# Performance work log

Hardware: AMD Instinct MI355X
Metric: run time of the kernel (lower is better)

Reference implementation:

```python
import jax, jax.numpy as jnp
import numpy as np

D = 256; H = 8; HD = D // H; L = 6; NQ = 100; DFF = 2048
FREQS = np.geomspace(1.0, 512.0, 10).astype(np.float32)  # WorldSpacePE: 10 freqs up to 512


def _ln(x, g, b, eps=1e-5):
    m = x.mean(-1, keepdims=True)
    v = ((x - m) ** 2).mean(-1, keepdims=True)
    return (x - m) * jax.lax.rsqrt(v + eps) * g + b


def _mha(q, k, v, Wq, bq, Wk, bk, Wv, bv, Wo, bo, bias=None):
    # standard nn.MultiheadAttention math (batch_first, eval mode -> no dropout)
    B, Q, _ = q.shape; N = k.shape[1]
    qh = (q @ Wq + bq).reshape(B, Q, H, HD).transpose(0, 2, 1, 3)
    kh = (k @ Wk + bk).reshape(B, N, H, HD).transpose(0, 2, 1, 3)
    vh = (v @ Wv + bv).reshape(B, N, H, HD).transpose(0, 2, 1, 3)
    s = jnp.einsum('bhqd,bhkd->bhqk', qh, kh) / np.float32(np.sqrt(HD))
    if bias is not None:
        s = s + bias
    a = jax.nn.softmax(s, axis=-1)
    o = jnp.einsum('bhqk,bhkd->bhqd', a, vh).transpose(0, 2, 1, 3).reshape(B, Q, D)
    return o @ Wo + bo


def setup_inputs() -> dict:
    key = jax.random.key(0)
    cnt = [0]
    def nk():
        cnt[0] += 1
        return jax.random.fold_in(key, cnt[0])
    def rn(shape, scale=0.02):
        return (jax.random.normal(nk(), shape) * scale).astype(jnp.float32)
    def zeros(shape):
        return jnp.zeros(shape, jnp.float32)
    def ones(shape):
        return jnp.ones(shape, jnp.float32)
    B, N, NT = 8, 4096, 32
    inp = {
        'image_feats': jax.random.normal(nk(), (B, N, D), jnp.float32),
        'text_feats': jax.random.normal(nk(), (B, NT, 256), jnp.float32),
        'pointmap': jax.random.normal(nk(), (B, N, 3), jnp.float32),
        'query_embed': rn((NQ, D)),
        'presence_tok': rn((1, D)),
        'text_proj_W': rn((256, D)), 'text_proj_b': zeros((D,)),
        'tWq': rn((D, D)), 'tbq': zeros((D,)), 'tWk': rn((D, D)), 'tbk': zeros((D,)),
        'tWv': rn((D, D)), 'tbv': zeros((D,)), 'tWo': rn((D, D)), 'tbo': zeros((D,)),
        'tln_g': ones((D,)), 'tln_b': zeros((D,)),
        'wpe_W': rn((60, D)), 'wpe_b': zeros((D,)),
        'sa_Wq': rn((L, D, D)), 'sa_bq': zeros((L, D)), 'sa_Wk': rn((L, D, D)), 'sa_bk': zeros((L, D)),
        'sa_Wv': rn((L, D, D)), 'sa_bv': zeros((L, D)), 'sa_Wo': rn((L, D, D)), 'sa_bo': zeros((L, D)),
        'ca_Wq': rn((L, D, D)), 'ca_bq': zeros((L, D)), 'ca_Wk': rn((L, D, D)), 'ca_bk': zeros((L, D)),
        'ca_Wv': rn((L, D, D)), 'ca_bv': zeros((L, D)), 'ca_Wo': rn((L, D, D)), 'ca_bo': zeros((L, D)),
        'ffn_W1': rn((L, D, DFF)), 'ffn_b1': zeros((L, DFF)),
        'ffn_W2': rn((L, DFF, D)), 'ffn_b2': zeros((L, D)),
        'ln1_g': ones((L, D)), 'ln1_b': zeros((L, D)),
        'ln2_g': ones((L, D)), 'ln2_b': zeros((L, D)),
        'ln3_g': ones((L, D)), 'ln3_b': zeros((L, D)),
        'pos_W': rn((L, D, 3)), 'pos_b': zeros((L, 3)),
        'beta': ones((L, H)),  # gasa_beta_init = 1.0
        'fin_g': ones((D,)), 'fin_b': zeros((D,)),
        'pW1': rn((D, D)), 'pb1': zeros((D,)),
        'pW2': rn((D, D)), 'pb2': zeros((D,)),
        'pW3': rn((D, 1)), 'pb3': zeros((1,)),
    }
    return inp


def reference(image_feats, text_feats, pointmap, query_embed, presence_tok,
              text_proj_W, text_proj_b,
              tWq, tbq, tWk, tbk, tWv, tbv, tWo, tbo, tln_g, tln_b,
              wpe_W, wpe_b,
              sa_Wq, sa_bq, sa_Wk, sa_bk, sa_Wv, sa_bv, sa_Wo, sa_bo,
              ca_Wq, ca_bq, ca_Wk, ca_bk, ca_Wv, ca_bv, ca_Wo, ca_bo,
              ffn_W1, ffn_b1, ffn_W2, ffn_b2,
              ln1_g, ln1_b, ln2_g, ln2_b, ln3_g, ln3_b,
              pos_W, pos_b, beta, fin_g, fin_b,
              pW1, pb1, pW2, pb2, pW3, pb3):
    B, N, _ = image_feats.shape
    # --- world-space PE from pointmap (sin/cos over 10 freqs, 3 coords -> 60d -> D) ---
    ang = pointmap[..., None] * jnp.asarray(FREQS)            # [B,N,3,10]
    enc = jnp.concatenate([jnp.sin(ang), jnp.cos(ang)], -1).reshape(B, N, 60)
    mem = image_feats + enc @ wpe_W + wpe_b                   # PE added to memory
    # --- text conditioning of queries ---
    txt = text_feats @ text_proj_W + text_proj_b              # [B,NT,D]
    x = jnp.concatenate([
        jnp.broadcast_to(query_embed, (B, NQ, D)),
        jnp.broadcast_to(presence_tok, (B, 1, D)),
    ], axis=1)                                                # [B,101,D]
    x = _ln(x + _mha(x, txt, txt, tWq, tbq, tWk, tbk, tWv, tbv, tWo, tbo), tln_g, tln_b)
    # --- decoder layers with GASA geometric attention bias (post-norm) ---
    for i in range(L):
        x = _ln(x + _mha(x, x, x, sa_Wq[i], sa_bq[i], sa_Wk[i], sa_bk[i],
                         sa_Wv[i], sa_bv[i], sa_Wo[i], sa_bo[i]), ln1_g[i], ln1_b[i])
        pos_q = x @ pos_W[i] + pos_b[i]                       # [B,101,3] predicted 3D pos
        d2 = jnp.sum((pos_q[:, :, None, :] - pointmap[:, None, :, :]) ** 2, -1)  # [B,101,N]
        bias = -jax.nn.softplus(beta[i])[None, :, None, None] * d2[:, None]      # [B,H,101,N]
        x = _ln(x + _mha(x, mem, mem, ca_Wq[i], ca_bq[i], ca_Wk[i], ca_bk[i],
                         ca_Wv[i], ca_bv[i], ca_Wo[i], ca_bo[i], bias=bias), ln2_g[i], ln2_b[i])
        h = jax.nn.relu(x @ ffn_W1[i] + ffn_b1[i]) @ ffn_W2[i] + ffn_b2[i]
        x = _ln(x + h, ln3_g[i], ln3_b[i])
    x = _ln(x, fin_g, fin_b)
    hs = x[:, :NQ]                                            # [B,100,D]
    pres = x[:, NQ]                                           # [B,D]
    h = jax.nn.relu(pres @ pW1 + pb1)
    h = jax.nn.relu(h @ pW2 + pb2)
    presence_logit = h @ pW3 + pb3                            # [B,1]
    return hs, presence_logit
```

## Files before the change

kernel.cpp:

```cpp
#include <hip/hip_runtime.h>
#include <math.h>

#define DD 256
#define NH 8
#define HDIM 32
#define NLAY 6
#define NQRY 100
#define TT 101
#define BB 8
#define NN 4096
#define NTXT 32
#define FFD 2048
#define MM (BB*TT)
#define MMP 896
#define BNN (BB*NN)
#define KC 8
#define KPC (NN/KC)
#define D2 (DD*DD)
#define C1S 0.25506807170842403f

typedef __bf16 bf16x8 __attribute__((ext_vector_type(8)));
typedef float f32x4v __attribute__((ext_vector_type(4)));
typedef unsigned int u32x4 __attribute__((ext_vector_type(4)));
typedef unsigned int u32x2 __attribute__((ext_vector_type(2)));

__device__ __forceinline__ ushort f2b(float f) {
  unsigned u = __builtin_bit_cast(unsigned, f);
  u += 0x7FFF + ((u >> 16) & 1);
  return (ushort)(u >> 16);
}
__device__ __forceinline__ unsigned pk2(float lo, float hi) {
  return (unsigned)f2b(lo) | ((unsigned)f2b(hi) << 16);
}
__device__ __forceinline__ f32x4v mfma16(bf16x8 a, bf16x8 b, f32x4v c) {
  return __builtin_amdgcn_mfma_f32_16x16x32_bf16(a, b, c, 0, 0, 0);
}

__device__ __forceinline__ void gemm_core(const ushort* __restrict__ A, size_t lda,
                                          const ushort* __restrict__ Bt, size_t ldb,
                                          int m0, int n0, int kBeg, int kEnd,
                                          char* AsB, char* BsB, int t,
                                          f32x4v acc[2][4]) {
  int w = t >> 6, l = t & 63, lq = l & 15, lg = l >> 4;
  int acol = (t & 7) * 8;
  for (int k0 = kBeg; k0 < kEnd; k0 += 64) {
    __syncthreads();
#pragma unroll
    for (int p = 0; p < 4; ++p) {
      int row = (t >> 3) + p * 32;
      u32x4 v = *(const u32x4*)(A + (size_t)(m0 + row) * lda + k0 + acol);
      *(u32x4*)(AsB + row * 128 + ((acol * 2) ^ ((row & 7) << 4))) = v;
    }
#pragma unroll
    for (int p = 0; p < 2; ++p) {
      int row = (t >> 3) + p * 32;
      u32x4 v = *(const u32x4*)(Bt + (size_t)(n0 + row) * ldb + k0 + acol);
      *(u32x4*)(BsB + row * 128 + ((acol * 2) ^ ((row & 7) << 4))) = v;
    }
    __syncthreads();
#pragma unroll
    for (int ks = 0; ks < 2; ++ks) {
      bf16x8 af[2], bfr[4];
#pragma unroll
      for (int mt = 0; mt < 2; ++mt) {
        int row = w * 32 + mt * 16 + lq;
        int kb = ks * 64 + lg * 16;
        af[mt] = __builtin_bit_cast(
            bf16x8, *(const u32x4*)(AsB + row * 128 + (kb ^ ((row & 7) << 4))));
      }
#pragma unroll
      for (int nt = 0; nt < 4; ++nt) {
        int row = nt * 16 + lq;
        int kb = ks * 64 + lg * 16;
        bfr[nt] = __builtin_bit_cast(
            bf16x8, *(const u32x4*)(BsB + row * 128 + (kb ^ ((row & 7) << 4))));
      }
#pragma unroll
      for (int mt = 0; mt < 2; ++mt)
#pragma unroll
        for (int nt = 0; nt < 4; ++nt) acc[mt][nt] = mfma16(af[mt], bfr[nt], acc[mt][nt]);
    }
  }
}

__global__ __launch_bounds__(256) void k_enc(const float* __restrict__ pm,
                                             ushort* __restrict__ encb) {
  int t = threadIdx.x;
  int row = blockIdx.x * 32 + (t >> 3);
  int kb = (t & 7) * 8;
  ushort o[8];
#pragma unroll
  for (int u = 0; u < 8; ++u) {
    int k = kb + u;
    float val = 0.f;
    if (k < 60) {
      int c = k / 20, jj = k % 20;
      float f = (float)(1 << (jj % 10));
      float a = pm[(size_t)row * 3 + c] * f;
      val = (jj < 10) ? sinf(a) : cosf(a);
    }
    o[u] = f2b(val);
  }
  *(u32x4*)(encb + (size_t)row * 64 + kb) = *(const u32x4*)o;
}

__global__ __launch_bounds__(256) void k_wpet(const float* __restrict__ wpeW,
                                              ushort* __restrict__ wpeT) {
  int n = blockIdx.x * 16 + (threadIdx.x >> 4);
  int k = (threadIdx.x & 15) * 4;
  ushort o[4];
#pragma unroll
  for (int u = 0; u < 4; ++u) {
    int kk = k + u;
    o[u] = (kk < 60) ? f2b(wpeW[(size_t)kk * DD + n]) : (ushort)0;
  }
  *(u32x2*)(wpeT + (size_t)n * 64 + k) = *(const u32x2*)o;
}

__global__ __launch_bounds__(256) void k_gemm_mem(const ushort* __restrict__ encb,
                                                  const ushort* __restrict__ wpeT,
                                                  const float* __restrict__ wpeb,
                                                  const float* __restrict__ img,
                                                  ushort* __restrict__ memb) {
  __shared__ __align__(16) char AsB[16384];
  __shared__ __align__(16) char BsB[8192];
  int m0 = blockIdx.x * 128, n0 = blockIdx.y * 64;
  f32x4v acc[2][4] = {};
  gemm_core(encb, 64, wpeT, 64, m0, n0, 0, 64, AsB, BsB, threadIdx.x, acc);
  int t = threadIdx.x, w = t >> 6, l = t & 63, lq = l & 15, lg = l >> 4;
#pragma unroll
  for (int nt = 0; nt < 4; ++nt) {
    int n = n0 + nt * 16 + lq;
    float bv = wpeb[n];
#pragma unroll
    for (int mt = 0; mt < 2; ++mt) {
      int rowg = m0 + w * 32 + mt * 16 + lg * 4;
      f32x4v a = acc[mt][nt];
#pragma unroll
      for (int r = 0; r < 4; ++r)
        memb[(size_t)(rowg + r) * DD + n] = f2b(a[r] + bv + img[(size_t)(rowg + r) * DD + n]);
    }
  }
}

struct T2BArgs {
  const float* fam[8];
  const float* single[5];
  const float* fW1; const float* fW2;
  ushort* wT; ushort* w1T; ushort* w2T;
};
__global__ __launch_bounds__(256) void k_t2b_all(T2BArgs a) {
  __shared__ ushort T[64][72];
  int id = blockIdx.x;
  const float* src; ushort* dst; int K, N, k0, n0;
  if (id < 768) {
    int fam = id / 96, rem = id % 96, mi = rem >> 4, ti = rem & 15;
    src = a.fam[fam] + (size_t)mi * D2;
    dst = a.wT + (size_t)(fam * 6 + mi) * D2;
    K = DD; N = DD; k0 = (ti >> 2) * 64; n0 = (ti & 3) * 64;
  } else if (id < 848) {
    int j = (id - 768) >> 4, ti = (id - 768) & 15;
    src = a.single[j];
    dst = a.wT + (size_t)(48 + j) * D2;
    K = DD; N = DD; k0 = (ti >> 2) * 64; n0 = (ti & 3) * 64;
  } else if (id < 1616) {
    int t2 = id - 848, mi = t2 >> 7, ti = t2 & 127;
    src = a.fW1 + (size_t)mi * DD * FFD;
    dst = a.w1T + (size_t)mi * DD * FFD;
    K = DD; N = FFD; k0 = (ti >> 5) * 64; n0 = (ti & 31) * 64;
  } else {
    int t2 = id - 1616, mi = t2 >> 7, ti = t2 & 127;
    src = a.fW2 + (size_t)mi * DD * FFD;
    dst = a.w2T + (size_t)mi * DD * FFD;
    K = FFD; N = DD; k0 = (ti >> 2) * 64; n0 = (ti & 3) * 64;
  }
  int t = threadIdx.x;
  int kk = t >> 4, nn4 = (t & 15) * 4;
#pragma unroll
  for (int p = 0; p < 4; ++p) {
    int krow = kk + p * 16;
    float4 v = *(const float4*)(src + (size_t)(k0 + krow) * N + n0 + nn4);
    T[nn4 + 0][krow] = f2b(v.x);
    T[nn4 + 1][krow] = f2b(v.y);
    T[nn4 + 2][krow] = f2b(v.z);
    T[nn4 + 3][krow] = f2b(v.w);
  }
  __syncthreads();
  int nn = t >> 3, kk8 = (t & 7) * 8;
#pragma unroll
  for (int p = 0; p < 2; ++p) {
    int nrow = nn + p * 32;
    u32x4 v = *(const u32x4*)(&T[nrow][kk8]);
    *(u32x4*)(dst + (size_t)(n0 + nrow) * K + k0 + kk8) = v;
  }
}

__global__ __launch_bounds__(256) void k_pm4(const float* __restrict__ pm,
                                             float4* __restrict__ pm4) {
  int i = blockIdx.x * 256 + threadIdx.x;
  float x = pm[(size_t)i * 3 + 0];
  float y = pm[(size_t)i * 3 + 1];
  float z = pm[(size_t)i * 3 + 2];
  float4 v;
  v.x = x; v.y = y; v.z = z; v.w = x * x + y * y + z * z;
  pm4[i] = v;
}

__global__ __launch_bounds__(256) void k_f2b(const float* __restrict__ in,
                                             ushort* __restrict__ out, int n) {
  int i = (blockIdx.x * 256 + threadIdx.x) * 4;
  if (i + 3 < n) {
    float4 v = *(const float4*)(in + i);
    out[i + 0] = f2b(v.x);
    out[i + 1] = f2b(v.y);
    out[i + 2] = f2b(v.z);
    out[i + 3] = f2b(v.w);
  }
}

template <int OM>
__global__ __launch_bounds__(256) void k_gemm_gen(const ushort* __restrict__ A,
                                                  const ushort* __restrict__ Bt,
                                                  const float* __restrict__ bias,
                                                  void* __restrict__ C, int Nc) {
  __shared__ __align__(16) char AsB[16384];
  __shared__ __align__(16) char BsB[8192];
  int m0 = blockIdx.x * 128, n0 = blockIdx.y * 64;
  f32x4v acc[2][4] = {};
  gemm_core(A, 256, Bt, 256, m0, n0, 0, 256, AsB, BsB, threadIdx.x, acc);
  int t = threadIdx.x, w = t >> 6, l = t & 63, lq = l & 15, lg = l >> 4;
#pragma unroll
  for (int nt = 0; nt < 4; ++nt) {
    int n = n0 + nt * 16 + lq;
    float bv = bias[n];
#pragma unroll
    for (int mt = 0; mt < 2; ++mt) {
      int rowg = m0 + w * 32 + mt * 16 + lg * 4;
      f32x4v a = acc[mt][nt];
      a[0] += bv; a[1] += bv; a[2] += bv; a[3] += bv;
      if (OM == 2) {
        a[0] = fmaxf(a[0], 0.f); a[1] = fmaxf(a[1], 0.f);
        a[2] = fmaxf(a[2], 0.f); a[3] = fmaxf(a[3], 0.f);
      }
      if (OM == 3) { a[0] *= C1S; a[1] *= C1S; a[2] *= C1S; a[3] *= C1S; }
      if (OM == 0) {
        float* Cf = (float*)C;
#pragma unroll
        for (int r = 0; r < 4; ++r) Cf[(size_t)(rowg + r) * Nc + n] = a[r];
      } else {
        ushort* Cb = (ushort*)C;
#pragma unroll
        for (int r = 0; r < 4; ++r) Cb[(size_t)(rowg + r) * Nc + n] = f2b(a[r]);
      }
    }
  }
}

__global__ __launch_bounds__(256) void k_gemm_qkv(
    const ushort* __restrict__ A, const ushort* __restrict__ Bq,
    const ushort* __restrict__ Bk, const ushort* __restrict__ Bv,
    const float* __restrict__ bq, const float* __restrict__ bk,
    const float* __restrict__ bv, ushort* __restrict__ Qb,
    ushort* __restrict__ Kbs, ushort* __restrict__ Vst) {
  __shared__ __align__(16) char AsB[16384];
  __shared__ __align__(16) char BsB[8192];
  int sel = blockIdx.y >> 2;
  int n0 = (blockIdx.y & 3) * 64;
  int m0 = blockIdx.x * 128;
  const ushort* Bt = sel == 0 ? Bq : (sel == 1 ? Bk : Bv);
  const float* bias = sel == 0 ? bq : (sel == 1 ? bk : bv);
  f32x4v acc[2][4] = {};
  gemm_core(A, 256, Bt, 256, m0, n0, 0, 256, AsB, BsB, threadIdx.x, acc);
  int t = threadIdx.x, w = t >> 6, l = t & 63, lq = l & 15, lg = l >> 4;
#pragma unroll
  for (int nt = 0; nt < 4; ++nt) {
    int n = n0 + nt * 16 + lq;
    float bvv = bias[n];
#pragma unroll
    for (int mt = 0; mt < 2; ++mt) {
      int rowg = m0 + w * 32 + mt * 16 + lg * 4;
      f32x4v a = acc[mt][nt];
      a[0] += bvv; a[1] += bvv; a[2] += bvv; a[3] += bvv;
      if (sel == 0) {
#pragma unroll
        for (int r = 0; r < 4; ++r) Qb[(size_t)(rowg + r) * DD + n] = f2b(a[r] * C1S);
      } else if (sel == 1) {
#pragma unroll
        for (int r = 0; r < 4; ++r) Kbs[(size_t)(rowg + r) * DD + n] = f2b(a[r]);
      } else {
        int h = n >> 5, dd = n & 31;
#pragma unroll
        for (int r = 0; r < 4; ++r) {
          int rg = rowg + r;
          if (rg < MM) {
            int b = rg / TT, tq = rg % TT;
            Vst[((size_t)((b * 8 + h) * 32 + dd)) * 128 + tq] = f2b(a[r]);
          }
        }
      }
    }
  }
}

template <int QPROJ>
__global__ __launch_bounds__(256) void k_gemm_o_ln(
    const ushort* __restrict__ A, const ushort* __restrict__ WoT,
    const float* __restrict__ bo, const float* __restrict__ xres,
    const float* __restrict__ g, const float* __restrict__ be,
    float* __restrict__ xout, ushort* __restrict__ xbout,
    const float* __restrict__ Wp, const float* __restrict__ bp,
    float* __restrict__ pqout) {
  __shared__ __align__(16) char AsB[8192];
  __shared__ __align__(16) char BsB[32768];
  int m0 = blockIdx.x * 64;
  int t = threadIdx.x, w = t >> 6, l = t & 63, lq = l & 15, lg = l >> 4;
  int acol = (t & 7) * 8;
  f32x4v acc[16] = {};
  for (int k0 = 0; k0 < 256; k0 += 64) {
    __syncthreads();
#pragma unroll
    for (int p = 0; p < 2; ++p) {
      int row = (t >> 3) + p * 32;
      u32x4 v = *(const u32x4*)(A + (size_t)(m0 + row) * 256 + k0 + acol);
      *(u32x4*)(AsB + row * 128 + ((acol * 2) ^ ((row & 7) << 4))) = v;
    }
#pragma unroll
    for (int p = 0; p < 8; ++p) {
      int row = (t >> 3) + p * 32;
      u32x4 v = *(const u32x4*)(WoT + (size_t)row * 256 + k0 + acol);
      *(u32x4*)(BsB + row * 128 + ((acol * 2) ^ ((row & 7) << 4))) = v;
    }
    __syncthreads();
#pragma unroll
    for (int ks = 0; ks < 2; ++ks) {
      int kb = ks * 64 + lg * 16;
      int arow = w * 16 + lq;
      bf16x8 af = __builtin_bit_cast(
          bf16x8, *(const u32x4*)(AsB + arow * 128 + (kb ^ ((arow & 7) << 4))));
#pragma unroll
      for (int nt = 0; nt < 16; ++nt) {
        int brow = nt * 16 + lq;
        bf16x8 bf = __builtin_bit_cast(
            bf16x8, *(const u32x4*)(BsB + brow * 128 + (kb ^ ((brow & 7) << 4))));
        acc[nt] = mfma16(af, bf, acc[nt]);
      }
    }
  }
  int rowb = m0 + w * 16 + lg * 4;
  float s[4] = {}, s2[4] = {};
#pragma unroll
  for (int nt = 0; nt < 16; ++nt) {
    int col = nt * 16 + lq;
    float bv = bo[col];
    f32x4v a = acc[nt];
#pragma unroll
    for (int r = 0; r < 4; ++r) {
      a[r] += bv + xres[(size_t)(rowb + r) * DD + col];
      s[r] += a[r];
      s2[r] += a[r] * a[r];
    }
    acc[nt] = a;
  }
#pragma unroll
  for (int r = 0; r < 4; ++r) {
#pragma unroll
    for (int o = 1; o < 16; o <<= 1) {
      s[r] += __shfl_xor(s[r], o, 64);
      s2[r] += __shfl_xor(s2[r], o, 64);
    }
  }
  float mu[4], inv[4];
#pragma unroll
  for (int r = 0; r < 4; ++r) {
    mu[r] = s[r] * (1.f / DD);
    float var = s2[r] * (1.f / DD) - mu[r] * mu[r];
    inv[r] = rsqrtf(var + 1e-5f);
  }
  float pp0[4] = {}, pp1[4] = {}, pp2[4] = {};
#pragma unroll
  for (int nt = 0; nt < 16; ++nt) {
    int col = nt * 16 + lq;
    float gd = g[col], bd = be[col];
    float w0 = 0.f, w1 = 0.f, w2 = 0.f;
    if (QPROJ) { w0 = Wp[col * 3]; w1 = Wp[col * 3 + 1]; w2 = Wp[col * 3 + 2]; }
#pragma unroll
    for (int r = 0; r < 4; ++r) {
      float ln = (acc[nt][r] - mu[r]) * inv[r] * gd + bd;
      xout[(size_t)(rowb + r) * DD + col] = ln;
      xbout[(size_t)(rowb + r) * DD + col] = f2b(ln);
      if (QPROJ) { pp0[r] += ln * w0; pp1[r] += ln * w1; pp2[r] += ln * w2; }
    }
  }
  if (QPROJ) {
#pragma unroll
    for (int r = 0; r < 4; ++r) {
#pragma unroll
      for (int o = 1; o < 16; o <<= 1) {
        pp0[r] += __shfl_xor(pp0[r], o, 64);
        pp1[r] += __shfl_xor(pp1[r], o, 64);
        pp2[r] += __shfl_xor(pp2[r], o, 64);
      }
      if (lq == 0) {
        pqout[(size_t)(rowb + r) * 3 + 0] = pp0[r] + bp[0];
        pqout[(size_t)(rowb + r) * 3 + 1] = pp1[r] + bp[1];
        pqout[(size_t)(rowb + r) * 3 + 2] = pp2[r] + bp[2];
      }
    }
  }
}

__global__ __launch_bounds__(256) void k_init_x(const float* __restrict__ qe,
                                                const float* __restrict__ pt,
                                                float* __restrict__ x,
                                                ushort* __restrict__ xb) {
  int r = blockIdx.x, d = threadIdx.x;
  int t = r % TT;
  float v = (t < NQRY) ? qe[t * DD + d] : pt[d];
  x[(size_t)r * DD + d] = v;
  xb[(size_t)r * DD + d] = f2b(v);
}

__global__ __launch_bounds__(128) void k_attn_small(const float* __restrict__ q,
                                                    const float* __restrict__ k,
                                                    const float* __restrict__ v,
                                                    ushort* __restrict__ out,
                                                    int NK) {
  int bh = blockIdx.x;
  int b = bh >> 3, h = bh & 7;
  __shared__ float Ks[TT][HDIM];
  __shared__ float Vs[TT][HDIM];
  for (int i = threadIdx.x; i < NK * HDIM; i += 128) {
    int n = i >> 5, j = i & 31;
    Ks[n][j] = k[(size_t)(b * NK + n) * DD + h * HDIM + j];
    Vs[n][j] = v[(size_t)(b * NK + n) * DD + h * HDIM + j];
  }
  __syncthreads();
  int t = threadIdx.x;
  if (t >= TT) return;
  float qv[HDIM];
  const float* qp = q + (size_t)(b * TT + t) * DD + h * HDIM;
#pragma unroll
  for (int j = 0; j < HDIM; ++j) qv[j] = qp[j];
  const float sc = 0.17677669529663687f * 1.4426950408889634f;
  float l = 0.f, acc[HDIM] = {};
  for (int n = 0; n < NK; ++n) {
    float s = 0.f;
#pragma unroll
    for (int j = 0; j < HDIM; ++j) s += qv[j] * Ks[n][j];
    float p = exp2f(s * sc);
    l += p;
#pragma unroll
    for (int j = 0; j < HDIM; ++j) acc[j] += p * Vs[n][j];
  }
  float inv = 1.f / l;
  ushort* op = out + (size_t)(b * TT + t) * DD + h * HDIM;
#pragma unroll
  for (int j = 0; j < HDIM; ++j) op[j] = f2b(acc[j] * inv);
}

__global__ __launch_bounds__(256) void k_self_mfma(const ushort* __restrict__ Qb,
                                                   const ushort* __restrict__ Kbs,
                                                   const ushort* __restrict__ Vst,
                                                   ushort* __restrict__ out) {
  int bh = blockIdx.x;
  int b = bh >> 3, h = bh & 7;
  int t = threadIdx.x, w = t >> 6, l = t & 63, lq = l & 15, lg = l >> 4;
  __shared__ ushort Plds[4][2][16][40];
  const f32x4v Z = {0.f, 0.f, 0.f, 0.f};
  bf16x8 qfb[2];
  f32x4v oacc[2][2] = {};
  float lsum[2] = {0.f, 0.f};
#pragma unroll
  for (int qi = 0; qi < 2; ++qi) {
    int qidx = (w * 2 + qi) * 16 + lq;
    int qc = qidx < TT ? qidx : TT - 1;
    qfb[qi] = __builtin_bit_cast(
        bf16x8, *(const u32x4*)(Qb + (size_t)(b * TT + qc) * DD + h * HDIM + lg * 8));
  }
  for (int kk = 0; kk < 128; kk += 32) {
    bf16x8 kf[2], vf[2];
#pragma unroll
    for (int t2 = 0; t2 < 2; ++t2) {
      int key = kk + t2 * 16 + lq;
      int kc2 = key < TT ? key : TT - 1;
      kf[t2] = __builtin_bit_cast(
          bf16x8, *(const u32x4*)(Kbs + (size_t)(b * TT + kc2) * DD + h * HDIM + lg * 8));
    }
#pragma unroll
    for (int dt = 0; dt < 2; ++dt)
      vf[dt] = __builtin_bit_cast(
          bf16x8, *(const u32x4*)(Vst + (size_t)(bh * 32 + dt * 16 + lq) * 128 + kk + lg * 8));
#pragma unroll
    for (int qi = 0; qi < 2; ++qi) {
      f32x4v s0 = mfma16(kf[0], qfb[qi], Z);
      f32x4v s1 = mfma16(kf[1], qfb[qi], Z);
      float p[2][4];
#pragma unroll
      for (int t2 = 0; t2 < 2; ++t2) {
#pragma unroll
        for (int r = 0; r < 4; ++r) {
          int kr = kk + t2 * 16 + lg * 4 + r;
          float sv = (t2 == 0) ? s0[r] : s1[r];
          p[t2][r] = (kr < TT) ? exp2f(sv) : 0.f;
        }
        lsum[qi] += (p[t2][0] + p[t2][1]) + (p[t2][2] + p[t2][3]);
      }
      u32x2 w0, w1;
      w0[0] = pk2(p[0][0], p[0][1]);
      w0[1] = pk2(p[0][2], p[0][3]);
      w1[0] = pk2(p[1][0], p[1][1]);
      w1[1] = pk2(p[1][2], p[1][3]);
      *(u32x2*)(&Plds[w][qi][lq][lg * 4]) = w0;
      *(u32x2*)(&Plds[w][qi][lq][16 + lg * 4]) = w1;
      bf16x8 pf = __builtin_bit_cast(bf16x8, *(const u32x4*)(&Plds[w][qi][lq][lg * 8]));
      oacc[qi][0] = mfma16(vf[0], pf, oacc[qi][0]);
      oacc[qi][1] = mfma16(vf[1], pf, oacc[qi][1]);
    }
  }
#pragma unroll
  for (int qi = 0; qi < 2; ++qi) {
    float lv = lsum[qi];
    lv += __shfl_xor(lv, 16, 64);
    lv += __shfl_xor(lv, 32, 64);
    float inv = 1.f / lv;
    int qidx = (w * 2 + qi) * 16 + lq;
    if (qidx < TT) {
      ushort* op = out + (size_t)(b * TT + qidx) * DD + h * HDIM;
#pragma unroll
      for (int dt = 0; dt < 2; ++dt)
#pragma unroll
        for (int r = 0; r < 4; ++r)
          op[dt * 16 + lg * 4 + r] = f2b(oacc[qi][dt][r] * inv);
    }
  }
}

__global__ __launch_bounds__(256) void k_gemm_kv(const ushort* __restrict__ A,
                                                 const ushort* __restrict__ Btk,
                                                 const ushort* __restrict__ Btv,
                                                 const float* __restrict__ bk,
                                                 const float* __restrict__ bv,
                                                 ushort* __restrict__ Kb,
                                                 ushort* __restrict__ Vt) {
  __shared__ __align__(16) char LB[34816];
  char* AsB = LB;
  char* BsB = LB + 16384;
  int isV = blockIdx.y >= 2;
  int n0 = (blockIdx.y & 1) * 128;
  int m0 = blockIdx.x * 128;
  const ushort* Bt = isV ? Btv : Btk;
  int t = threadIdx.x, w = t >> 6, l = t & 63, lq = l & 15, lg = l >> 4;
  int acol = (t & 7) * 8;
  f32x4v acc[2][8] = {};
  for (int k0 = 0; k0 < 256; k0 += 64) {
    __syncthreads();
#pragma unroll
    for (int p = 0; p < 4; ++p) {
      int row = (t >> 3) + p * 32;
      u32x4 va = *(const u32x4*)(A + (size_t)(m0 + row) * 256 + k0 + acol);
      *(u32x4*)(AsB + row * 128 + ((acol * 2) ^ ((row & 7) << 4))) = va;
      u32x4 vb = *(const u32x4*)(Bt + (size_t)(n0 + row) * 256 + k0 + acol);
      *(u32x4*)(BsB + row * 128 + ((acol * 2) ^ ((row & 7) << 4))) = vb;
    }
    __syncthreads();
#pragma unroll
    for (int ks = 0; ks < 2; ++ks) {
      int kb = ks * 64 + lg * 16;
      bf16x8 af[2], bfr[8];
#pragma unroll
      for (int mt = 0; mt < 2; ++mt) {
        int row = w * 32 + mt * 16 + lq;
        af[mt] = __builtin_bit_cast(
            bf16x8, *(const u32x4*)(AsB + row * 128 + (kb ^ ((row & 7) << 4))));
      }
#pragma unroll
      for (int nt = 0; nt < 8; ++nt) {
        int row = nt * 16 + lq;
        bfr[nt] = __builtin_bit_cast(
            bf16x8, *(const u32x4*)(BsB + row * 128 + (kb ^ ((row & 7) << 4))));
      }
#pragma unroll
      for (int mt = 0; mt < 2; ++mt)
#pragma unroll
        for (int nt = 0; nt < 8; ++nt) acc[mt][nt] = mfma16(af[mt], bfr[nt], acc[mt][nt]);
    }
  }
  if (!isV) {
#pragma unroll
    for (int nt = 0; nt < 8; ++nt) {
      int n = n0 + nt * 16 + lq;
      float bvv = bk[n];
#pragma unroll
      for (int mt = 0; mt < 2; ++mt) {
        int rowg = m0 + w * 32 + mt * 16 + lg * 4;
        f32x4v a = acc[mt][nt];
#pragma unroll
        for (int r = 0; r < 4; ++r) Kb[(size_t)(rowg + r) * DD + n] = f2b(a[r] + bvv);
      }
    }
  } else {
    ushort* T = (ushort*)LB;
    __syncthreads();
#pragma unroll
    for (int nt = 0; nt < 8; ++nt) {
      int ddl = nt * 16 + lq;
      float bvv = bv[n0 + ddl];
#pragma unroll
      for (int mt = 0; mt < 2; ++mt) {
        int kl = w * 32 + mt * 16 + lg * 4;
        f32x4v a = acc[mt][nt];
        u32x2 pv;
        pv[0] = pk2(a[0] + bvv, a[1] + bvv);
        pv[1] = pk2(a[2] + bvv, a[3] + bvv);
        *(u32x2*)(T + ddl * 136 + kl) = pv;
      }
    }
    __syncthreads();
    int row = t >> 1, half = t & 1;
    int b = m0 >> 12, key0 = m0 & 4095;
    const ushort* src = T + row * 136 + half * 64;
    ushort* dst = Vt + ((size_t)(b * 256 + n0 + row)) * 4096 + key0 + half * 64;
#pragma unroll
    for (int i = 0; i < 8; ++i)
      *(u32x4*)(dst + i * 8) = *(const u32x4*)(src + i * 8);
  }
}

__global__ __launch_bounds__(256) void k_ffn2sk(const ushort* __restrict__ A,
                                                const ushort* __restrict__ Bt,
                                                float* __restrict__ P) {
  __shared__ __align__(16) char AsB[16384];
  __shared__ __align__(16) char BsB[8192];
  int m0 = blockIdx.x * 128, n0 = blockIdx.y * 64, z = blockIdx.z;
  f32x4v acc[2][4] = {};
  gemm_core(A, FFD, Bt, FFD, m0, n0, z * 256, z * 256 + 256, AsB, BsB, threadIdx.x, acc);
  int t = threadIdx.x, w = t >> 6, l = t & 63, lq = l & 15, lg = l >> 4;
#pragma unroll
  for (int nt = 0; nt < 4; ++nt) {
    int n = n0 + nt * 16 + lq;
#pragma unroll
    for (int mt = 0; mt < 2; ++mt) {
      int rowg = m0 + w * 32 + mt * 16 + lg * 4;
      f32x4v a = acc[mt][nt];
#pragma unroll
      for (int r = 0; r < 4; ++r)
        P[((size_t)z * MMP + rowg + r) * DD + n] = a[r];
    }
  }
}

__global__ __launch_bounds__(256) void k_red_ln3(const float* __restrict__ P,
                                                 const float* __restrict__ bias,
                                                 const float* __restrict__ xres,
                                                 const float* __restrict__ g,
                                                 const float* __restrict__ be,
                                                 float* __restrict__ xout,
                                                 ushort* __restrict__ xbout) {
  int row = blockIdx.x, d = threadIdx.x;
  float a = xres[(size_t)row * DD + d] + bias[d];
#pragma unroll
  for (int z = 0; z < 8; ++z) a += P[((size_t)z * MMP + row) * DD + d];
  float s = a, s2 = a * a;
#pragma unroll
  for (int o = 1; o < 64; o <<= 1) {
    s += __shfl_xor(s, o, 64);
    s2 += __shfl_xor(s2, o, 64);
  }
  __shared__ float ws[4], ws2[4];
  int wid = d >> 6;
  if ((d & 63) == 0) { ws[wid] = s; ws2[wid] = s2; }
  __syncthreads();
  s = ws[0] + ws[1] + ws[2] + ws[3];
  s2 = ws2[0] + ws2[1] + ws2[2] + ws2[3];
  float m = s * (1.f / DD);
  float var = s2 * (1.f / DD) - m * m;
  float inv = rsqrtf(var + 1e-5f);
  float r_ = (a - m) * inv * g[d] + be[d];
  xout[(size_t)row * DD + d] = r_;
  xbout[(size_t)row * DD + d] = f2b(r_);
}

__global__ __launch_bounds__(256) void k_cross_mfma(
    const ushort* __restrict__ Qb, const ushort* __restrict__ Kb,
    const ushort* __restrict__ Vt, const float* __restrict__ posq,
    const float4* __restrict__ pm4, const float* __restrict__ betaL,
    float* __restrict__ pacc, float* __restrict__ pl) {
  int bh = blockIdx.x, kc = blockIdx.y;
  int b = bh >> 3, h = bh & 7;
  int t = threadIdx.x, w = t >> 6, l = t & 63, lq = l & 15, lg = l >> 4;
  const float L2E = 1.4426950408889634f;
  float spb = log1pf(expf(betaL[h]));
  float cb = spb * L2E;

  __shared__ float4 pm4s[KPC];
  __shared__ ushort Plds[4][2][16][40];

  int kbase = b * NN + kc * KPC;
  for (int i = t; i < KPC; i += 256) pm4s[i] = pm4[kbase + i];
  __syncthreads();

  const f32x4v Z = {0.f, 0.f, 0.f, 0.f};
  bf16x8 qfb[2];
  float a0[2], px[2], py[2], pz[2];
  f32x4v oacc[2][2] = {};
  float lsum[2] = {0.f, 0.f};

#pragma unroll
  for (int qi = 0; qi < 2; ++qi) {
    int qt = w * 2 + qi;
    int qidx = qt * 16 + lq;
    int qc = qidx < TT ? qidx : TT - 1;
    size_t xr = (size_t)(b * TT + qc);
    qfb[qi] = __builtin_bit_cast(
        bf16x8, *(const u32x4*)(Qb + xr * 256 + h * 32 + lg * 8));
    float qx = posq[xr * 3 + 0], qy = posq[xr * 3 + 1], qz = posq[xr * 3 + 2];
    a0[qi] = -cb * (qx * qx + qy * qy + qz * qz);
    px[qi] = 2.f * cb * qx;
    py[qi] = 2.f * cb * qy;
    pz[qi] = 2.f * cb * qz;
  }

  for (int kk = 0; kk < KPC; kk += 32) {
    bf16x8 kf[2], vf[2];
#pragma unroll
    for (int t2 = 0; t2 < 2; ++t2)
      kf[t2] = __builtin_bit_cast(
          bf16x8, *(const u32x4*)(Kb + (size_t)(kbase + kk + t2 * 16 + lq) * 256 +
                                  h * 32 + lg * 8));
#pragma unroll
    for (int dt = 0; dt < 2; ++dt)
      vf[dt] = __builtin_bit_cast(
          bf16x8, *(const u32x4*)(Vt + (size_t)(bh * 32 + dt * 16 + lq) * 4096 +
                                  kc * KPC + kk + lg * 8));
    float bx[2][4], by[2][4], bz[2][4], b0[2][4];
#pragma unroll
    for (int t2 = 0; t2 < 2; ++t2)
#pragma unroll
      for (int r = 0; r < 4; ++r) {
        float4 pv = pm4s[kk + t2 * 16 + lg * 4 + r];
        bx[t2][r] = pv.x; by[t2][r] = pv.y; bz[t2][r] = pv.z;
        b0[t2][r] = cb * pv.w;
      }
#pragma unroll
    for (int qi = 0; qi < 2; ++qi) {
      f32x4v s0 = mfma16(kf[0], qfb[qi], Z);
      f32x4v s1 = mfma16(kf[1], qfb[qi], Z);
      float p[2][4];
#pragma unroll
      for (int t2 = 0; t2 < 2; ++t2) {
#pragma unroll
        for (int r = 0; r < 4; ++r) {
          float sv = (t2 == 0) ? s0[r] : s1[r];
          float bias = fmaf(px[qi], bx[t2][r],
                       fmaf(py[qi], by[t2][r],
                       fmaf(pz[qi], bz[t2][r], a0[qi] - b0[t2][r])));
          p[t2][r] = exp2f(sv + bias);
        }
        lsum[qi] += (p[t2][0] + p[t2][1]) + (p[t2][2] + p[t2][3]);
      }
      u32x2 w0, w1;
      w0[0] = pk2(p[0][0], p[0][1]);
      w0[1] = pk2(p[0][2], p[0][3]);
      w1[0] = pk2(p[1][0], p[1][1]);
      w1[1] = pk2(p[1][2], p[1][3]);
      *(u32x2*)(&Plds[w][qi][lq][lg * 4]) = w0;
      *(u32x2*)(&Plds[w][qi][lq][16 + lg * 4]) = w1;
      bf16x8 pf = __builtin_bit_cast(bf16x8, *(const u32x4*)(&Plds[w][qi][lq][lg * 8]));
      oacc[qi][0] = mfma16(vf[0], pf, oacc[qi][0]);
      oacc[qi][1] = mfma16(vf[1], pf, oacc[qi][1]);
    }
  }

#pragma unroll
  for (int qi = 0; qi < 2; ++qi) {
    float lv = lsum[qi];
    lv += __shfl_xor(lv, 16, 64);
    lv += __shfl_xor(lv, 32, 64);
// ... 45 lines not shown
  }
  __shared__ float ws[4], ws2[4];
  int wid = d >> 6;
  if ((d & 63) == 0) { ws[wid] = s; ws2[wid] = s2; }
  __syncthreads();
  s = ws[0] + ws[1] + ws[2] + ws[3];
  s2 = ws2[0] + ws2[1] + ws2[2] + ws2[3];
  float m = s * (1.f / DD);
  float var = s2 * (1.f / DD) - m * m;
  float inv = rsqrtf(var + 1e-5f);
  float r = (v - m) * inv * g[d] + be[d];
  if (tq < NQRY) hs[((size_t)(b * NQRY + tq)) * DD + d] = r;
  else pres[(size_t)b * DD + d] = r;
}

__global__ __launch_bounds__(256) void k_mlp8(const float* __restrict__ in,
                                              const float* __restrict__ W,
                                              const float* __restrict__ b,
                                              float* __restrict__ out) {
  __shared__ float ins[8][DD];
  __shared__ float red[8][32][8];
  int t = threadIdx.x;
  for (int i = t; i < 8 * DD; i += 256) ins[i >> 8][i & 255] = in[i];
  __syncthreads();
  int c = t & 31, ks = t >> 5;
  int cg = blockIdx.x * 32 + c;
  float acc[8] = {};
  for (int k = ks * 32; k < ks * 32 + 32; ++k) {
    float w = W[(size_t)k * DD + cg];
#pragma unroll
    for (int r = 0; r < 8; ++r) acc[r] += ins[r][k] * w;
  }
#pragma unroll
  for (int r = 0; r < 8; ++r) red[ks][c][r] = acc[r];
  __syncthreads();
  int c2 = t & 31, r2 = t >> 5;
  float s = 0.f;
#pragma unroll
  for (int k2 = 0; k2 < 8; ++k2) s += red[k2][c2][r2];
  s = fmaxf(s + b[blockIdx.x * 32 + c2], 0.f);
  out[(size_t)r2 * DD + blockIdx.x * 32 + c2] = s;
}

__global__ __launch_bounds__(256) void k_logit(const float* __restrict__ h2,
                                               const float* __restrict__ W3,
                                               const float* __restrict__ b3,
                                               float* __restrict__ out) {
  int r = threadIdx.x >> 5, lane = threadIdx.x & 31;
  float s = 0.f;
  for (int k = lane; k < DD; k += 32) s += h2[r * DD + k] * W3[k];
#pragma unroll
  for (int o = 16; o; o >>= 1) s += __shfl_xor(s, o, 32);
  if (lane == 0) out[r] = s + b3[0];
}

extern "C" void kernel_launch(void* const* d_in, const int* in_sizes, int n_in,
                              void* d_out, int out_size, void* d_ws, size_t ws_size,
                              hipStream_t stream) {
  (void)in_sizes; (void)n_in; (void)out_size; (void)ws_size;
  auto F = [&](int i) { return (const float*)d_in[i]; };
  const float* img   = F(0);
  const float* txtf  = F(1);
  const float* pm    = F(2);
  const float* qe    = F(3);
  const float* ptok  = F(4);
  const float* tpW   = F(5);
  const float* tpb   = F(6);
  const float* tWq   = F(7);  const float* tbq = F(8);
  const float* tWk   = F(9);  const float* tbk = F(10);
  const float* tWv   = F(11); const float* tbv = F(12);
  const float* tWo   = F(13); const float* tbo = F(14);
  const float* tlng  = F(15); const float* tlnb = F(16);
  const float* wpeW  = F(17); const float* wpeb = F(18);
  const float* saWq  = F(19); const float* sabq = F(20);
  const float* saWk  = F(21); const float* sabk = F(22);
  const float* saWv  = F(23); const float* sabv = F(24);
  const float* saWo  = F(25); const float* sabo = F(26);
  const float* caWq  = F(27); const float* cabq = F(28);
  const float* caWk  = F(29); const float* cabk = F(30);
  const float* caWv  = F(31); const float* cabv = F(32);
  const float* caWo  = F(33); const float* cabo = F(34);
  const float* fW1   = F(35); const float* fb1 = F(36);
  const float* fW2   = F(37); const float* fb2 = F(38);
  const float* ln1g  = F(39); const float* ln1b = F(40);
  const float* ln2g  = F(41); const float* ln2b = F(42);
  const float* ln3g  = F(43); const float* ln3b = F(44);
  const float* posW  = F(45); const float* posb = F(46);
  const float* beta  = F(47);
  const float* fing  = F(48); const float* finb = F(49);
  const float* pW1   = F(50); const float* pb1 = F(51);
  const float* pW2   = F(52); const float* pb2 = F(53);
  const float* pW3   = F(54); const float* pb3 = F(55);

  char* wp = (char*)d_ws;
  auto alloc = [&](size_t bytes) {
    char* p = wp;
    wp += (bytes + 255) & ~(size_t)255;
    return (void*)p;
  };
  ushort* memb = (ushort*)alloc((size_t)BNN * DD * 2);
  ushort* Kb   = (ushort*)alloc((size_t)BNN * DD * 2);
  ushort* Vt   = (ushort*)alloc((size_t)64 * 32 * 4096 * 2);
  ushort* encb = (ushort*)alloc((size_t)BNN * 64 * 2);
  ushort* wT   = (ushort*)alloc((size_t)53 * D2 * 2);
  ushort* w1T  = (ushort*)alloc((size_t)6 * FFD * DD * 2);
  ushort* w2T  = (ushort*)alloc((size_t)6 * DD * FFD * 2);
  ushort* xb   = (ushort*)alloc((size_t)MMP * DD * 2);
  ushort* hb   = (ushort*)alloc((size_t)MMP * FFD * 2);
  ushort* tDb  = (ushort*)alloc((size_t)MMP * DD * 2);
  ushort* tQb  = (ushort*)alloc((size_t)MMP * DD * 2);
  ushort* tKb  = (ushort*)alloc((size_t)MMP * DD * 2);
  ushort* tQb2 = (ushort*)alloc((size_t)MMP * DD * 2);
  ushort* Vst  = (ushort*)alloc((size_t)64 * 32 * 128 * 2);
  ushort* txtb = (ushort*)alloc((size_t)BB * NTXT * DD * 2);
  ushort* txtb2= (ushort*)alloc((size_t)BB * NTXT * DD * 2);
  float* fp2  = (float*)alloc((size_t)8 * MMP * DD * 4);
  float* x    = (float*)alloc((size_t)MMP * DD * 4);
  float* tA   = (float*)alloc((size_t)MMP * DD * 4);
  float* tK   = (float*)alloc((size_t)BB * NTXT * DD * 4);
  float* tV   = (float*)alloc((size_t)BB * NTXT * DD * 4);
  float* pacc = (float*)alloc((size_t)(KC * 64 + 8) * TT * HDIM * 4);
  float* pl   = (float*)alloc((size_t)(KC * 64 + 8) * TT * 4);
  float* posq = (float*)alloc((size_t)4096 * 4);
  float4* pm4 = (float4*)alloc((size_t)BNN * 16);
  float* pres = (float*)alloc((size_t)BB * DD * 4);
  float* ph1  = (float*)alloc((size_t)BB * DD * 4);
  float* ph2  = (float*)alloc((size_t)BB * DD * 4);
  ushort* wpeT = (ushort*)alloc((size_t)DD * 64 * 2);

  k_enc<<<BNN / 32, 256, 0, stream>>>(pm, encb);
  k_wpet<<<16, 256, 0, stream>>>(wpeW, wpeT);
  k_pm4<<<BNN / 256, 256, 0, stream>>>(pm, pm4);
  T2BArgs ta;
  ta.fam[0] = saWq; ta.fam[1] = saWk; ta.fam[2] = saWv; ta.fam[3] = saWo;
  ta.fam[4] = caWq; ta.fam[5] = caWk; ta.fam[6] = caWv; ta.fam[7] = caWo;
  ta.single[0] = tpW; ta.single[1] = tWq; ta.single[2] = tWk;
  ta.single[3] = tWv; ta.single[4] = tWo;
  ta.fW1 = fW1; ta.fW2 = fW2; ta.wT = wT; ta.w1T = w1T; ta.w2T = w2T;
  k_t2b_all<<<2384, 256, 0, stream>>>(ta);
  k_gemm_mem<<<dim3(256, 4), 256, 0, stream>>>(encb, wpeT, wpeb, img, memb);

  k_f2b<<<(BB * NTXT * DD) / 1024, 256, 0, stream>>>(txtf, txtb, BB * NTXT * DD);
  k_gemm_gen<1><<<dim3(2, 4), 256, 0, stream>>>(txtb, wT + (size_t)48 * D2, tpb, txtb2, DD);
  k_gemm_gen<0><<<dim3(2, 4), 256, 0, stream>>>(txtb2, wT + (size_t)50 * D2, tbk, tK, DD);
  k_gemm_gen<0><<<dim3(2, 4), 256, 0, stream>>>(txtb2, wT + (size_t)51 * D2, tbv, tV, DD);
  k_init_x<<<MM, 256, 0, stream>>>(qe, ptok, x, xb);
  k_gemm_gen<0><<<dim3(7, 4), 256, 0, stream>>>(xb, wT + (size_t)49 * D2, tbq, tA, DD);
  k_attn_small<<<64, 128, 0, stream>>>(tA, tK, tV, tDb, NTXT);
  k_gemm_o_ln<0><<<14, 256, 0, stream>>>(tDb, wT + (size_t)52 * D2, tbo, x, tlng, tlnb,
                                         x, xb, nullptr, nullptr, nullptr);

  for (int i = 0; i < NLAY; ++i) {
    int iD = i * DD;
    k_gemm_qkv<<<dim3(7, 12), 256, 0, stream>>>(
        xb, wT + (size_t)(0 + i) * D2, wT + (size_t)(6 + i) * D2, wT + (size_t)(12 + i) * D2,
        sabq + iD, sabk + iD, sabv + iD, tQb, tKb, Vst);
    k_self_mfma<<<64, 256, 0, stream>>>(tQb, tKb, Vst, tDb);
    k_gemm_o_ln<1><<<14, 256, 0, stream>>>(tDb, wT + (size_t)(18 + i) * D2, sabo + iD,
                                           x, ln1g + iD, ln1b + iD, x, xb,
                                           posW + (size_t)i * DD * 3, posb + i * 3, posq);
    k_gemm_gen<3><<<dim3(7, 4), 256, 0, stream>>>(xb, wT + (size_t)(24 + i) * D2,
                                                  cabq + iD, tQb2, DD);
    k_gemm_kv<<<dim3(256, 4), 256, 0, stream>>>(memb, wT + (size_t)(30 + i) * D2,
                                                wT + (size_t)(36 + i) * D2,
                                                cabk + iD, cabv + iD, Kb, Vt);
    k_cross_mfma<<<dim3(64, KC), 256, 0, stream>>>(tQb2, Kb, Vt, posq, pm4,
                                                   beta + i * NH, pacc, pl);
    k_cross_merge<<<dim3(64, 13), 256, 0, stream>>>(pacc, pl, tDb);
    k_gemm_o_ln<0><<<14, 256, 0, stream>>>(tDb, wT + (size_t)(42 + i) * D2, cabo + iD,
                                           x, ln2g + iD, ln2b + iD, x, xb,
                                           nullptr, nullptr, nullptr);
    k_gemm_gen<2><<<dim3(7, 32), 256, 0, stream>>>(xb, w1T + (size_t)i * DD * FFD,
                                                   fb1 + i * FFD, hb, FFD);
    k_ffn2sk<<<dim3(7, 4, 8), 256, 0, stream>>>(hb, w2T + (size_t)i * DD * FFD, fp2);
    k_red_ln3<<<MM, 256, 0, stream>>>(fp2, fb2 + iD, x, ln3g + iD, ln3b + iD, x, xb);
  }

  k_fin<<<MM, 256, 0, stream>>>(x, fing, finb, (float*)d_out, pres);
  k_mlp8<<<8, 256, 0, stream>>>(pres, pW1, pb1, ph1);
  k_mlp8<<<8, 256, 0, stream>>>(ph1, pW2, pb2, ph2);
  k_logit<<<1, 256, 0, stream>>>(ph2, pW3, pb3, (float*)d_out + (size_t)BB * NQRY * DD);
}
```

Measured before the change: 858.1 us.

## Use direct global-to-LDS loads and merge self-QKV with cross K/V GEMM launch

GEMM tile staging now uses global_load_lds 16-byte async loads with the XOR swizzle applied on the source address, avoiding the round trip through registers. The self-attention QKV projection and the per-layer memory K/V projection are fused into one kernel launch whose block index selects the role. The memory K/V work is independent of x, so it fills the GPU alongside the small QKV GEMM and removes one launch per layer. This adds reliance on the gfx950 LDS-direct load path and a heterogeneous kernel with shared LDS sizing.

```diff
diff --git a/kernel.cpp b/kernel.cpp
--- a/kernel.cpp
+++ b/kernel.cpp
@@ -36,27 +36,39 @@
   return __builtin_amdgcn_mfma_f32_16x16x32_bf16(a, b, c, 0, 0, 0);
 }
 
+__device__ __forceinline__ void gload16(const void* g, void* l) {
+  __builtin_amdgcn_global_load_lds(
+      (const __attribute__((address_space(1))) void*)g,
+      (__attribute__((address_space(3))) void*)l, 16, 0, 0);
+}
+
+template <int NROWS>
+__device__ __forceinline__ void stage_sw(const ushort* __restrict__ G, size_t ldg,
+                                         int row0, int k0, char* lds, int w, int l) {
+  constexpr int RPW = NROWS / 4;
+  constexpr int ISSUES = RPW / 8;
+#pragma unroll
+  for (int p = 0; p < ISSUES; ++p) {
+    int slot = p * 64 + l;
+    int row = w * RPW + (slot >> 3);
+    int blk = slot & 7;
+    int cb = blk ^ (row & 7);
+    const ushort* src = G + (size_t)(row0 + row) * ldg + (size_t)k0 + cb * 8;
+    char* db = lds + (w * RPW + p * 8) * 128;
+    gload16(src, db);
+  }
+}
+
 __device__ __forceinline__ void gemm_core(const ushort* __restrict__ A, size_t lda,
                                           const ushort* __restrict__ Bt, size_t ldb,
                                           int m0, int n0, int kBeg, int kEnd,
                                           char* AsB, char* BsB, int t,
                                           f32x4v acc[2][4]) {
   int w = t >> 6, l = t & 63, lq = l & 15, lg = l >> 4;
-  int acol = (t & 7) * 8;
   for (int k0 = kBeg; k0 < kEnd; k0 += 64) {
     __syncthreads();
-#pragma unroll
-    for (int p = 0; p < 4; ++p) {
-      int row = (t >> 3) + p * 32;
-      u32x4 v = *(const u32x4*)(A + (size_t)(m0 + row) * lda + k0 + acol);
-      *(u32x4*)(AsB + row * 128 + ((acol * 2) ^ ((row & 7) << 4))) = v;
-    }
-#pragma unroll
-    for (int p = 0; p < 2; ++p) {
-      int row = (t >> 3) + p * 32;
-      u32x4 v = *(const u32x4*)(Bt + (size_t)(n0 + row) * ldb + k0 + acol);
-      *(u32x4*)(BsB + row * 128 + ((acol * 2) ^ ((row & 7) << 4))) = v;
-    }
+    stage_sw<128>(A, lda, m0, k0, AsB, w, l);
+    stage_sw<64>(Bt, ldb, n0, k0, BsB, w, l);
     __syncthreads();
 #pragma unroll
     for (int ks = 0; ks < 2; ++ks) {
@@ -256,48 +268,133 @@
   }
 }
 
-__global__ __launch_bounds__(256) void k_gemm_qkv(
-    const ushort* __restrict__ A, const ushort* __restrict__ Bq,
+__global__ __launch_bounds__(256) void k_qkv_kv(
+    const ushort* __restrict__ xbA, const ushort* __restrict__ Bq,
     const ushort* __restrict__ Bk, const ushort* __restrict__ Bv,
     const float* __restrict__ bq, const float* __restrict__ bk,
     const float* __restrict__ bv, ushort* __restrict__ Qb,
-    ushort* __restrict__ Kbs, ushort* __restrict__ Vst) {
-  __shared__ __align__(16) char AsB[16384];
-  __shared__ __align__(16) char BsB[8192];
-  int sel = blockIdx.y >> 2;
-  int n0 = (blockIdx.y & 3) * 64;
-  int m0 = blockIdx.x * 128;
-  const ushort* Bt = sel == 0 ? Bq : (sel == 1 ? Bk : Bv);
-  const float* bias = sel == 0 ? bq : (sel == 1 ? bk : bv);
-  f32x4v acc[2][4] = {};
-  gemm_core(A, 256, Bt, 256, m0, n0, 0, 256, AsB, BsB, threadIdx.x, acc);
+    ushort* __restrict__ Kbs, ushort* __restrict__ Vst,
+    const ushort* __restrict__ memb, const ushort* __restrict__ Btk,
+    const ushort* __restrict__ Btv, const float* __restrict__ cbk,
+    const float* __restrict__ cbv, ushort* __restrict__ Kb,
+    ushort* __restrict__ Vt) {
+  __shared__ __align__(16) char LB[34816];
+  int bid = blockIdx.x;
   int t = threadIdx.x, w = t >> 6, l = t & 63, lq = l & 15, lg = l >> 4;
-#pragma unroll
-  for (int nt = 0; nt < 4; ++nt) {
-    int n = n0 + nt * 16 + lq;
-    float bvv = bias[n];
-#pragma unroll
-    for (int mt = 0; mt < 2; ++mt) {
-      int rowg = m0 + w * 32 + mt * 16 + lg * 4;
-      f32x4v a = acc[mt][nt];
-      a[0] += bvv; a[1] += bvv; a[2] += bvv; a[3] += bvv;
-      if (sel == 0) {
-#pragma unroll
-        for (int r = 0; r < 4; ++r) Qb[(size_t)(rowg + r) * DD + n] = f2b(a[r] * C1S);
-      } else if (sel == 1) {
-#pragma unroll
-        for (int r = 0; r < 4; ++r) Kbs[(size_t)(rowg + r) * DD + n] = f2b(a[r]);
-      } else {
-        int h = n >> 5, dd = n & 31;
-#pragma unroll
-        for (int r = 0; r < 4; ++r) {
-          int rg = rowg + r;
-          if (rg < MM) {
-            int b = rg / TT, tq = rg % TT;
-            Vst[((size_t)((b * 8 + h) * 32 + dd)) * 128 + tq] = f2b(a[r]);
+  if (bid < 84) {
+    char* AsB = LB;
+    char* BsB = LB + 16384;
+    int m0 = (bid % 7) * 128;
+    int yy = bid / 7;
+    int sel = yy >> 2;
+    int n0 = (yy & 3) * 64;
+    const ushort* Bt = sel == 0 ? Bq : (sel == 1 ? Bk : Bv);
+    const float* bias = sel == 0 ? bq : (sel == 1 ? bk : bv);
+    f32x4v acc[2][4] = {};
+    gemm_core(xbA, 256, Bt, 256, m0, n0, 0, 256, AsB, BsB, t, acc);
+#pragma unroll
+    for (int nt = 0; nt < 4; ++nt) {
+      int n = n0 + nt * 16 + lq;
+      float bvv = bias[n];
+#pragma unroll
+      for (int mt = 0; mt < 2; ++mt) {
+        int rowg = m0 + w * 32 + mt * 16 + lg * 4;
+        f32x4v a = acc[mt][nt];
+        a[0] += bvv; a[1] += bvv; a[2] += bvv; a[3] += bvv;
+        if (sel == 0) {
+#pragma unroll
+          for (int r = 0; r < 4; ++r) Qb[(size_t)(rowg + r) * DD + n] = f2b(a[r] * C1S);
+        } else if (sel == 1) {
+#pragma unroll
+          for (int r = 0; r < 4; ++r) Kbs[(size_t)(rowg + r) * DD + n] = f2b(a[r]);
+        } else {
+          int h = n >> 5, dd = n & 31;
+#pragma unroll
+          for (int r = 0; r < 4; ++r) {
+            int rg = rowg + r;
+            if (rg < MM) {
+              int b = rg / TT, tq = rg % TT;
+              Vst[((size_t)((b * 8 + h) * 32 + dd)) * 128 + tq] = f2b(a[r]);
+            }
           }
         }
       }
+    }
+  } else {
+    char* AsB = LB;
+    char* BsB = LB + 16384;
+    int tile = bid - 84;
+    int m0 = (tile & 255) * 128;
+    int yy = tile >> 8;
+    int isV = yy >= 2;
+    int n0 = (yy & 1) * 128;
+    const ushort* Bt = isV ? Btv : Btk;
+    f32x4v acc[2][8] = {};
+    for (int k0 = 0; k0 < 256; k0 += 64) {
+      __syncthreads();
+      stage_sw<128>(memb, 256, m0, k0, AsB, w, l);
+      stage_sw<128>(Bt, 256, n0, k0, BsB, w, l);
+      __syncthreads();
+#pragma unroll
+      for (int ks = 0; ks < 2; ++ks) {
+        int kb = ks * 64 + lg * 16;
+        bf16x8 af[2], bfr[8];
+#pragma unroll
+        for (int mt = 0; mt < 2; ++mt) {
+          int row = w * 32 + mt * 16 + lq;
+          af[mt] = __builtin_bit_cast(
+              bf16x8, *(const u32x4*)(AsB + row * 128 + (kb ^ ((row & 7) << 4))));
+        }
+#pragma unroll
+        for (int nt = 0; nt < 8; ++nt) {
+          int row = nt * 16 + lq;
+          bfr[nt] = __builtin_bit_cast(
+              bf16x8, *(const u32x4*)(BsB + row * 128 + (kb ^ ((row & 7) << 4))));
+        }
+#pragma unroll
+        for (int mt = 0; mt < 2; ++mt)
+#pragma unroll
+          for (int nt = 0; nt < 8; ++nt) acc[mt][nt] = mfma16(af[mt], bfr[nt], acc[mt][nt]);
+      }
+    }
+    if (!isV) {
+#pragma unroll
+      for (int nt = 0; nt < 8; ++nt) {
+        int n = n0 + nt * 16 + lq;
+        float bvv = cbk[n];
+#pragma unroll
+        for (int mt = 0; mt < 2; ++mt) {
+          int rowg = m0 + w * 32 + mt * 16 + lg * 4;
+          f32x4v a = acc[mt][nt];
+#pragma unroll
+          for (int r = 0; r < 4; ++r) Kb[(size_t)(rowg + r) * DD + n] = f2b(a[r] + bvv);
+        }
+      }
+    } else {
+      ushort* T = (ushort*)LB;
+      __syncthreads();
+#pragma unroll
+      for (int nt = 0; nt < 8; ++nt) {
+        int ddl = nt * 16 + lq;
+        float bvv = cbv[n0 + ddl];
+#pragma unroll
+        for (int mt = 0; mt < 2; ++mt) {
+          int kl = w * 32 + mt * 16 + lg * 4;
+          f32x4v a = acc[mt][nt];
+          u32x2 pv;
+          pv[0] = pk2(a[0] + bvv, a[1] + bvv);
+          pv[1] = pk2(a[2] + bvv, a[3] + bvv);
+          *(u32x2*)(T + ddl * 136 + kl) = pv;
+        }
+      }
+      __syncthreads();
+      int row = t >> 1, half = t & 1;
+      int b = m0 >> 12, key0 = m0 & 4095;
+      const ushort* src = T + row * 136 + half * 64;
+      ushort* dst = Vt + ((size_t)(b * 256 + n0 + row)) * 4096 + key0 + half * 64;
+#pragma unroll
+      for (int i = 0; i < 8; ++i)
+        *(u32x4*)(dst + i * 8) = *(const u32x4*)(src + i * 8);
     }
   }
 }
@@ -314,22 +411,11 @@
   __shared__ __align__(16) char BsB[32768];
   int m0 = blockIdx.x * 64;
   int t = threadIdx.x, w = t >> 6, l = t & 63, lq = l & 15, lg = l >> 4;
-  int acol = (t & 7) * 8;
   f32x4v acc[16] = {};
   for (int k0 = 0; k0 < 256; k0 += 64) {
     __syncthreads();
-#pragma unroll
-    for (int p = 0; p < 2; ++p) {
-      int row = (t >> 3) + p * 32;
-      u32x4 v = *(const u32x4*)(A + (size_t)(m0 + row) * 256 + k0 + acol);
-      *(u32x4*)(AsB + row * 128 + ((acol * 2) ^ ((row & 7) << 4))) = v;
-    }
-#pragma unroll
-    for (int p = 0; p < 8; ++p) {
-      int row = (t >> 3) + p * 32;
-      u32x4 v = *(const u32x4*)(WoT + (size_t)row * 256 + k0 + acol);
-      *(u32x4*)(BsB + row * 128 + ((acol * 2) ^ ((row & 7) << 4))) = v;
-    }
+    stage_sw<64>(A, 256, m0, k0, AsB, w, l);
+    stage_sw<256>(WoT, 256, 0, k0, BsB, w, l);
     __syncthreads();
 #pragma unroll
     for (int ks = 0; ks < 2; ++ks) {
@@ -532,97 +618,6 @@
         for (int r = 0; r < 4; ++r)
           op[dt * 16 + lg * 4 + r] = f2b(oacc[qi][dt][r] * inv);
     }
-  }
-}
-
-__global__ __launch_bounds__(256) void k_gemm_kv(const ushort* __restrict__ A,
-                                                 const ushort* __restrict__ Btk,
-                                                 const ushort* __restrict__ Btv,
-                                                 const float* __restrict__ bk,
-                                                 const float* __restrict__ bv,
-                                                 ushort* __restrict__ Kb,
-                                                 ushort* __restrict__ Vt) {
-  __shared__ __align__(16) char LB[34816];
-  char* AsB = LB;
-  char* BsB = LB + 16384;
-  int isV = blockIdx.y >= 2;
-  int n0 = (blockIdx.y & 1) * 128;
-  int m0 = blockIdx.x * 128;
-  const ushort* Bt = isV ? Btv : Btk;
-  int t = threadIdx.x, w = t >> 6, l = t & 63, lq = l & 15, lg = l >> 4;
-  int acol = (t & 7) * 8;
-  f32x4v acc[2][8] = {};
-  for (int k0 = 0; k0 < 256; k0 += 64) {
-    __syncthreads();
-#pragma unroll
-    for (int p = 0; p < 4; ++p) {
-      int row = (t >> 3) + p * 32;
-      u32x4 va = *(const u32x4*)(A + (size_t)(m0 + row) * 256 + k0 + acol);
-      *(u32x4*)(AsB + row * 128 + ((acol * 2) ^ ((row & 7) << 4))) = va;
-      u32x4 vb = *(const u32x4*)(Bt + (size_t)(n0 + row) * 256 + k0 + acol);
-      *(u32x4*)(BsB + row * 128 + ((acol * 2) ^ ((row & 7) << 4))) = vb;
-    }
-    __syncthreads();
-#pragma unroll
-    for (int ks = 0; ks < 2; ++ks) {
-      int kb = ks * 64 + lg * 16;
-      bf16x8 af[2], bfr[8];
-#pragma unroll
-      for (int mt = 0; mt < 2; ++mt) {
-        int row = w * 32 + mt * 16 + lq;
-        af[mt] = __builtin_bit_cast(
-            bf16x8, *(const u32x4*)(AsB + row * 128 + (kb ^ ((row & 7) << 4))));
-      }
-#pragma unroll
-      for (int nt = 0; nt < 8; ++nt) {
-        int row = nt * 16 + lq;
-        bfr[nt] = __builtin_bit_cast(
-            bf16x8, *(const u32x4*)(BsB + row * 128 + (kb ^ ((row & 7) << 4))));
-      }
-#pragma unroll
-      for (int mt = 0; mt < 2; ++mt)
-#pragma unroll
-        for (int nt = 0; nt < 8; ++nt) acc[mt][nt] = mfma16(af[mt], bfr[nt], acc[mt][nt]);
-    }
-  }
-  if (!isV) {
-#pragma unroll
-    for (int nt = 0; nt < 8; ++nt) {
-      int n = n0 + nt * 16 + lq;
-      float bvv = bk[n];
-#pragma unroll
-      for (int mt = 0; mt < 2; ++mt) {
-        int rowg = m0 + w * 32 + mt * 16 + lg * 4;
-        f32x4v a = acc[mt][nt];
-#pragma unroll
-        for (int r = 0; r < 4; ++r) Kb[(size_t)(rowg + r) * DD + n] = f2b(a[r] + bvv);
-      }
-    }
-  } else {
-    ushort* T = (ushort*)LB;
-    __syncthreads();
-#pragma unroll
-    for (int nt = 0; nt < 8; ++nt) {
-      int ddl = nt * 16 + lq;
-      float bvv = bv[n0 + ddl];
-#pragma unroll
-      for (int mt = 0; mt < 2; ++mt) {
-        int kl = w * 32 + mt * 16 + lg * 4;
-        f32x4v a = acc[mt][nt];
-        u32x2 pv;
-        pv[0] = pk2(a[0] + bvv, a[1] + bvv);
-        pv[1] = pk2(a[2] + bvv, a[3] + bvv);
-        *(u32x2*)(T + ddl * 136 + kl) = pv;
-      }
-    }
-    __syncthreads();
-    int row = t >> 1, half = t & 1;
-    int b = m0 >> 12, key0 = m0 & 4095;
-    const ushort* src = T + row * 136 + half * 64;
-    ushort* dst = Vt + ((size_t)(b * 256 + n0 + row)) * 4096 + key0 + half * 64;
-#pragma unroll
-    for (int i = 0; i < 8; ++i)
-      *(u32x4*)(dst + i * 8) = *(const u32x4*)(src + i * 8);
   }
 }
 
@@ -974,18 +969,17 @@
 
   for (int i = 0; i < NLAY; ++i) {
     int iD = i * DD;
-    k_gemm_qkv<<<dim3(7, 12), 256, 0, stream>>>(
+    k_qkv_kv<<<1108, 256, 0, stream>>>(
         xb, wT + (size_t)(0 + i) * D2, wT + (size_t)(6 + i) * D2, wT + (size_t)(12 + i) * D2,
-        sabq + iD, sabk + iD, sabv + iD, tQb, tKb, Vst);
+        sabq + iD, sabk + iD, sabv + iD, tQb, tKb, Vst,
+        memb, wT + (size_t)(30 + i) * D2, wT + (size_t)(36 + i) * D2,
+        cabk + iD, cabv + iD, Kb, Vt);
     k_self_mfma<<<64, 256, 0, stream>>>(tQb, tKb, Vst, tDb);
     k_gemm_o_ln<1><<<14, 256, 0, stream>>>(tDb, wT + (size_t)(18 + i) * D2, sabo + iD,
                                            x, ln1g + iD, ln1b + iD, x, xb,
                                            posW + (size_t)i * DD * 3, posb + i * 3, posq);
     k_gemm_gen<3><<<dim3(7, 4), 256, 0, stream>>>(xb, wT + (size_t)(24 + i) * D2,
                                                   cabq + iD, tQb2, DD);
-    k_gemm_kv<<<dim3(256, 4), 256, 0, stream>>>(memb, wT + (size_t)(30 + i) * D2,
-                                                wT + (size_t)(36 + i) * D2,
-                                                cabk + iD, cabv + iD, Kb, Vt);
     k_cross_mfma<<<dim3(64, KC), 256, 0, stream>>>(tQb2, Kb, Vt, posq, pm4,
                                                    beta + i * NH, pacc, pl);
     k_cross_merge<<<dim3(64, 13), 256, 0, stream>>>(pacc, pl, tDb);
```

Result: faster. 710.6 us (-17.2%).
